# Kernel optimization log

Hardware: AMD Instinct MI355X
Metric: run time of the kernel (lower is better)

Reference implementation:

```python
import jax, jax.numpy as jnp
import numpy as np
from jax import lax

B, S, V, E, H, NH = 32, 512, 30000, 300, 200, 4
ENC = 2 * H           # bidirectional encoder size = 400
DH = ENC // NH        # head dim = 100
BUDGET = 20.0         # percent of length kept by sparseMAP
SCALING = 1.0 / 0.001 # eval-mode temperature (module sets 0.001 at test time)
NEG = -1e9


def setup_inputs():
    key = jax.random.key(0)
    ks = jax.random.split(key, 16)
    lengths = jax.random.randint(ks[0], (B,), S // 2, S + 1)
    mask = jnp.arange(S)[None, :] < lengths[:, None]          # prefix mask [B,S]
    x = jax.random.randint(ks[1], (B, S), 0, V)
    p = lambda k, sh: jax.random.normal(k, sh, jnp.float32) * 0.05
    return {
        "x": x, "mask": mask,
        "embed_table": p(ks[2], (V, E)),
        "w_ih_f": p(ks[3], (4 * H, E)), "w_hh_f": p(ks[4], (4 * H, H)), "b_f": jnp.zeros((4 * H,), jnp.float32),
        "w_ih_b": p(ks[5], (4 * H, E)), "w_hh_b": p(ks[6], (4 * H, H)), "b_b": jnp.zeros((4 * H,), jnp.float32),
        "q_state": p(ks[7], (ENC,)),
        "W_q": p(ks[8], (ENC, ENC)), "W_k": p(ks[9], (ENC, ENC)), "W_v": p(ks[10], (ENC, ENC)),
        "W_out": p(ks[11], (ENC, ENC)),
        "W_head": p(ks[12], (ENC, 1)), "b_head": jnp.zeros((1,), jnp.float32),
    }


def _lstm(xW, mask, W_hh):
    """Masked (packed-equivalent) LSTM. xW: [B,S,4H] precomputed input proj, mask [B,S] bool."""
    Bb, Ss, H4 = xW.shape
    Hh = H4 // 4
    def step(carry, t_in):
        h, c = carry
        g, m = t_in                             # g [B,4H], m [B,1] bool
        gates = g + h @ W_hh.T
        i, f, gg, o = jnp.split(gates, 4, axis=-1)
        c_new = jax.nn.sigmoid(f) * c + jax.nn.sigmoid(i) * jnp.tanh(gg)
        h_new = jax.nn.sigmoid(o) * jnp.tanh(c_new)
        return (jnp.where(m, h_new, h), jnp.where(m, c_new, c)), jnp.where(m, h_new, 0.0)
    init = (jnp.zeros((Bb, Hh), xW.dtype), jnp.zeros((Bb, Hh), xW.dtype))
    xs = (jnp.swapaxes(xW, 0, 1), jnp.swapaxes(mask[..., None], 0, 1))
    _, outs = lax.scan(step, init, xs)
    return jnp.swapaxes(outs, 0, 1)


def _proj_capped_simplex(theta, k):
    """SparseMAP budget QP: argmin ||mu - theta||^2 s.t. 0<=mu<=1, sum(mu)=k.
    Bisection on threshold tau (non-diff), then exact differentiable tau on the free set."""
    th = lax.stop_gradient(theta)
    lo = jnp.min(th) - 1.0
    hi = jnp.max(th)
    def body(_, ab):
        lo, hi = ab
        mid = 0.5 * (lo + hi)
        too_big = jnp.sum(jnp.clip(th - mid, 0.0, 1.0)) > k
        return (jnp.where(too_big, mid, lo), jnp.where(too_big, hi, mid))
    lo, hi = lax.fori_loop(0, 60, body, (lo, hi))
    tau0 = 0.5 * (lo + hi)
    mu0 = th - tau0
    free = (mu0 > 0.0) & (mu0 < 1.0)
    nU = jnp.sum(mu0 >= 1.0).astype(theta.dtype)
    nS = jnp.sum(free).astype(theta.dtype)
    tau = (jnp.sum(jnp.where(free, theta, 0.0)) + nU - k) / jnp.maximum(nS, 1.0)
    tau = jnp.where(nS > 0, tau, tau0)
    return jnp.clip(theta - tau, 0.0, 1.0)


def _forward(x, mask, embed_table, w_ih_f, w_hh_f, b_f, w_ih_b, w_hh_b, b_b,
             q_state, W_q, W_k, W_v, W_out, W_head, b_head):
    lengths = mask.sum(1)                                   # [B] int
    emb = embed_table[x]                                    # [B,S,E] (dropout off: eval)
    # forward direction
    h_f = _lstm(emb @ w_ih_f.T + b_f, mask, w_hh_f)         # [B,S,H]
    # backward direction: reverse each sample within its length (packed semantics)
    t = jnp.arange(S)
    idx = jnp.clip(lengths[:, None] - 1 - t[None, :], 0, S - 1)   # [B,S], involution on valid part
    emb_rev = jnp.take_along_axis(emb, idx[..., None], axis=1)
    h_b_rev = _lstm(emb_rev @ w_ih_b.T + b_b, mask, w_hh_b)
    h_b = jnp.take_along_axis(h_b_rev, idx[..., None], axis=1)
    h_b = jnp.where(mask[..., None], h_b, 0.0)
    h = jnp.concatenate([h_f, h_b], axis=-1)                # [B,S,ENC]
    # Hopfield pooling with learned query state, per-sample sparseMAP top-k budget
    q = (q_state @ W_q).reshape(NH, DH)                     # learned pooling query
    K = (h @ W_k).reshape(B, S, NH, DH)
    Vv = (h @ W_v).reshape(B, S, NH, DH)
    scores = SCALING * jnp.einsum('hd,bshd->bhs', q, K)     # [B,NH,S]
    scores = jnp.where(mask[:, None, :], scores, NEG)
    kbud = jnp.round(BUDGET / 100.0 * lengths.astype(jnp.float32))   # per-sample budget
    proj = jax.vmap(jax.vmap(_proj_capped_simplex, (0, None)), (0, 0))
    p = proj(scores, kbud)                                  # [B,NH,S] sparse marginals
    pooled = jnp.einsum('bhs,bshd->bhd', p, Vv).reshape(B, ENC) @ W_out
    y = jax.nn.sigmoid(pooled @ W_head + b_head)            # [B,1]
    z = jnp.where(mask, p.mean(1), 0.0)                     # [B,S] rationale
    return y, z


def reference(x, mask, embed_table, w_ih_f, w_hh_f, b_f, w_ih_b, w_hh_b, b_b,
              q_state, W_q, W_k, W_v, W_out, W_head, b_head):
    return _forward(x, mask, embed_table, w_ih_f, w_hh_f, b_f, w_ih_b, w_hh_b, b_b,
                    q_state, W_q, W_k, W_v, W_out, W_head, b_head)
```

## Files before the change

### kernel.cpp

```cpp
#include <hip/hip_runtime.h>
#include <hip/hip_bf16.h>
#include <math.h>

#define B_   32
#define S_   512
#define V_   30000
#define E_   300
#define H_   200
#define NH_  4
#define ENC_ 400
#define G4_  800
#define NEGV  (-1e9f)
#define SCALE_ 1000.0f

typedef _Float16 half2v __attribute__((ext_vector_type(2)));

#if defined(__has_builtin)
#if __has_builtin(__builtin_amdgcn_fdot2)
#define FDOT2(a,b,c) __builtin_amdgcn_fdot2((a),(b),(c),false)
#endif
#endif
#ifndef FDOT2
#define FDOT2(a,b,c) fmaf((float)(a)[1],(float)(b)[1], fmaf((float)(a)[0],(float)(b)[0],(c)))
#endif

#define OF_QVEC  320000ull
#define OF_WKQ   320448ull
#define OF_THETA 322048ull
#define OF_MU    387584ull
#define OF_HP    453120ull
#define OF_LEN   504320ull
#define OF_XWF   504384ull
#define OF_XWB   13611584ull
#define OF_HF    26718784ull
#define OF_HB    29995584ull

__global__ void k_lengths(const void* __restrict__ mask, int* __restrict__ lengths) {
  int b = blockIdx.x, lane = threadIdx.x;
  const unsigned char* mb = (const unsigned char*)mask;
  int mode;
  if (mb[1] != 0) mode = 0;
  else if (((const int*)mask)[1] != 0) mode = 1;
  else mode = 2;
  int cnt = 0;
  for (int s = lane; s < S_; s += 64) {
    int v;
    if (mode == 0)      v = mb[b*S_ + s] ? 1 : 0;
    else if (mode == 1) v = ((const int*)mask)[b*S_ + s] ? 1 : 0;
    else                v = ((const long long*)mask)[b*S_ + s] ? 1 : 0;
    cnt += v;
  }
  for (int off = 32; off; off >>= 1) cnt += __shfl_xor(cnt, off);
  if (lane == 0) lengths[b] = cnt;
}

__global__ void k_qvec(const float* __restrict__ qs, const float* __restrict__ Wq,
                       float* __restrict__ qvec) {
  __shared__ float qsl[ENC_];
  int t = threadIdx.x;
  if (t < ENC_) qsl[t] = qs[t];
  __syncthreads();
  if (t < ENC_) {
    float acc = 0.f;
    for (int i = 0; i < ENC_; ++i) acc += qsl[i] * Wq[(size_t)i*ENC_ + t];
    qvec[t] = acc;
  }
}

__global__ void k_wkq(const float* __restrict__ Wk, const float* __restrict__ qvec,
                      float* __restrict__ wkq) {
  int t = threadIdx.x;
  int e = blockIdx.x*64 + (t >> 2);
  int head = t & 3;
  if (e < ENC_) {
    float acc = 0.f;
    const float* row = Wk + (size_t)e*ENC_ + head*100;
    const float* qv  = qvec + head*100;
    for (int d = 0; d < 100; ++d) acc += row[d]*qv[d];
    wkq[e*4 + head] = acc;
  }
}

__global__ __launch_bounds__(256) void k_gemm_in(
    const int* __restrict__ x, const float* __restrict__ emb,
    const float* __restrict__ wf, const float* __restrict__ wb,
    const float* __restrict__ bf, const float* __restrict__ bb,
    float* __restrict__ xWf, float* __restrict__ xWb)
{
  __shared__ int xid[128];
  __shared__ __align__(16) float sA[16][128];
  __shared__ __align__(16) float sB[16][64];
  const int t = threadIdx.x;
  const int row0 = blockIdx.x * 128;
  const int col0 = blockIdx.y * 64;
  if (t < 128) xid[t] = x[row0 + t];
  __syncthreads();
  float acc[8][4];
  #pragma unroll
  for (int i = 0; i < 8; ++i)
    #pragma unroll
    for (int j = 0; j < 4; ++j) acc[i][j] = 0.f;
  const int y = t >> 4, xq = t & 15;
  const int rl = t >> 1, half = t & 1;
  const int cb = t & 63, kq = t >> 6;
  const int colg_b = col0 + cb;
  const float* wsrc = (colg_b < 800) ? (wf + (size_t)colg_b*300)
                                     : (wb + (size_t)(colg_b-800)*300);
  const float* asrc = emb + (size_t)xid[rl]*300;
  for (int kc = 0; kc < 19; ++kc) {
    const int k0 = kc*16;
    {
      const int kb = k0 + half*8;
      const float* src = asrc + kb;
      if (kb + 7 < 300) {
        float4 a  = *(const float4*)(src);
        float4 b4 = *(const float4*)(src+4);
        sA[half*8+0][rl]=a.x;  sA[half*8+1][rl]=a.y;  sA[half*8+2][rl]=a.z;  sA[half*8+3][rl]=a.w;
        sA[half*8+4][rl]=b4.x; sA[half*8+5][rl]=b4.y; sA[half*8+6][rl]=b4.z; sA[half*8+7][rl]=b4.w;
      } else {
        #pragma unroll
        for (int i = 0; i < 8; ++i) sA[half*8+i][rl] = (kb+i < 300) ? src[i] : 0.f;
      }
    }
    {
      const int kb = k0 + kq*4;
      if (kb + 3 < 300) {
        float4 w4 = *(const float4*)(wsrc + kb);
        sB[kq*4+0][cb]=w4.x; sB[kq*4+1][cb]=w4.y; sB[kq*4+2][cb]=w4.z; sB[kq*4+3][cb]=w4.w;
      } else {
        #pragma unroll
        for (int i = 0; i < 4; ++i) sB[kq*4+i][cb] = (kb+i < 300) ? wsrc[kb+i] : 0.f;
      }
    }
    __syncthreads();
    #pragma unroll
    for (int k = 0; k < 16; ++k) {
      float4 a0 = *(const float4*)&sA[k][y*8];
      float4 a1 = *(const float4*)&sA[k][y*8+4];
      float4 b4 = *(const float4*)&sB[k][xq*4];
      float av[8] = {a0.x,a0.y,a0.z,a0.w,a1.x,a1.y,a1.z,a1.w};
      float bv[4] = {b4.x,b4.y,b4.z,b4.w};
      #pragma unroll
      for (int i = 0; i < 8; ++i)
        #pragma unroll
        for (int j = 0; j < 4; ++j) acc[i][j] += av[i]*bv[j];
    }
    __syncthreads();
  }
  const int colg = col0 + xq*4;
  const bool isF = (colg < 800);
  const int colo = isF ? colg : (colg - 800);
  float4 bias = isF ? *(const float4*)(bf + colo) : *(const float4*)(bb + colo);
  float* dst = isF ? xWf : xWb;
  #pragma unroll
  for (int i = 0; i < 8; ++i) {
    int row = row0 + y*8 + i;
    float4 o = {acc[i][0]+bias.x, acc[i][1]+bias.y, acc[i][2]+bias.z, acc[i][3]+bias.w};
    *(float4*)(dst + (size_t)row*800 + colo) = o;
  }
}

__global__ __launch_bounds__(512, 2) void k_lstm_ws(
    const float* __restrict__ xWf, const float* __restrict__ xWb,
    const float* __restrict__ whhf, const float* __restrict__ whhb,
    const int* __restrict__ lengths,
    float* __restrict__ h_f, float* __restrict__ h_b)
{
  const int bid = blockIdx.x;
  const int dir = bid >> 5, b = bid & 31;
  const float* __restrict__ xW  = dir ? xWb : xWf;
  const float* __restrict__ whh = dir ? whhb : whhf;
  float* __restrict__ hout      = dir ? h_b : h_f;
  const int len = lengths[b];
  const int t = threadIdx.x;

  __shared__ __align__(16) _Float16 hb[256];
  __shared__ float sums[1024];

  half2v w0[100], w1[100];
  {
    const float* r0p = whh + (size_t)t*H_;
    #pragma unroll
    for (int j = 0; j < 50; ++j) {
      float4 a = *(const float4*)(r0p + 4*j);
      w0[2*j]   = half2v{(_Float16)a.x, (_Float16)a.y};
      w0[2*j+1] = half2v{(_Float16)a.z, (_Float16)a.w};
    }
    if (t < 288) {
      const float* r1p = whh + (size_t)(512+t)*H_;
      #pragma unroll
      for (int j = 0; j < 50; ++j) {
        float4 a = *(const float4*)(r1p + 4*j);
        w1[2*j]   = half2v{(_Float16)a.x, (_Float16)a.y};
        w1[2*j+1] = half2v{(_Float16)a.z, (_Float16)a.w};
      }
    } else {
      #pragma unroll
      for (int j = 0; j < 100; ++j) w1[j] = half2v{(_Float16)0.f, (_Float16)0.f};
    }
  }

  if (t < 256) hb[t] = (_Float16)0.f;
  float cst = 0.f;
  __syncthreads();

  for (int step = 0; step < len; ++step) {
    const int pos = dir ? (len-1-step) : step;
    float xi=0.f, xf=0.f, xg=0.f, xo=0.f;
    if (t < H_) {
      const float* xr = xW + ((size_t)b*S_ + pos)*G4_ + t;
      xi = xr[0]; xf = xr[H_]; xg = xr[2*H_]; xo = xr[3*H_];
    }
    float a0 = 0.f, a1 = 0.f;
    #pragma unroll
    for (int j = 0; j < 25; ++j) {
      float4 h4 = *(const float4*)&hb[8*j];
      half2v p0 = __builtin_bit_cast(half2v, h4.x);
      half2v p1 = __builtin_bit_cast(half2v, h4.y);
      half2v p2 = __builtin_bit_cast(half2v, h4.z);
      half2v p3 = __builtin_bit_cast(half2v, h4.w);
      a0 = FDOT2(w0[4*j],   p0, a0);
      a0 = FDOT2(w0[4*j+1], p1, a0);
      a0 = FDOT2(w0[4*j+2], p2, a0);
      a0 = FDOT2(w0[4*j+3], p3, a0);
      a1 = FDOT2(w1[4*j],   p0, a1);
      a1 = FDOT2(w1[4*j+1], p1, a1);
      a1 = FDOT2(w1[4*j+2], p2, a1);
      a1 = FDOT2(w1[4*j+3], p3, a1);
    }
    sums[t] = a0;
    sums[512+t] = a1;
    __syncthreads();
    if (t < H_) {
      float gi = sums[t]        + xi;
      float gf = sums[H_ + t]   + xf;
      float gg = sums[2*H_ + t] + xg;
      float go = sums[3*H_ + t] + xo;
      float ig = 1.f/(1.f+__expf(-gi));
      float fg = 1.f/(1.f+__expf(-gf));
      float og = 1.f/(1.f+__expf(-go));
      float ggc = fminf(fmaxf(gg, -10.f), 10.f);
      float eg = __expf(2.f*ggc);
      cst = fg*cst + ig*((eg-1.f)/(eg+1.f));
      float cc = fminf(fmaxf(cst, -10.f), 10.f);
      float ec = __expf(2.f*cc);
      float hn = og*((ec-1.f)/(ec+1.f));
      hout[((size_t)b*S_ + pos)*H_ + t] = hn;
      hb[t] = (_Float16)hn;
    }
    __syncthreads();
  }
}

__global__ __launch_bounds__(256) void k_scores(
    const float* __restrict__ hf, const float* __restrict__ hb,
    const float* __restrict__ wkq, const int* __restrict__ lengths,
    float* __restrict__ theta)
{
  int wid = blockIdx.x*4 + (threadIdx.x >> 6);
  int lane = threadIdx.x & 63;
  int b = wid >> 9, s = wid & 511;
  const float* hfr = hf + ((size_t)b*S_ + s)*H_;
  const float* hbr = hb + ((size_t)b*S_ + s)*H_;
  float a0=0.f, a1=0.f, a2=0.f, a3=0.f;
  for (int e = lane; e < ENC_; e += 64) {
    float hv = (e < H_) ? hfr[e] : hbr[e-H_];
    float4 w = *(const float4*)(wkq + e*4);
    a0 += hv*w.x; a1 += hv*w.y; a2 += hv*w.z; a3 += hv*w.w;
  }
  for (int off = 32; off; off >>= 1) {
    a0 += __shfl_xor(a0, off); a1 += __shfl_xor(a1, off);
    a2 += __shfl_xor(a2, off); a3 += __shfl_xor(a3, off);
  }
  if (lane == 0) {
    bool valid = s < lengths[b];
    size_t base = (size_t)b*2048 + s;
    theta[base       ] = valid ? SCALE_*a0 : NEGV;
    theta[base +  512] = valid ? SCALE_*a1 : NEGV;
    theta[base + 1024] = valid ? SCALE_*a2 : NEGV;
    theta[base + 1536] = valid ? SCALE_*a3 : NEGV;
  }
}

__global__ void k_sparsemap(const float* __restrict__ theta, const int* __restrict__ lengths,
                            float* __restrict__ mu) {
  int pid = blockIdx.x;
  int lane = threadIdx.x;
  const float* th = theta + (size_t)pid*512;
  float v[8];
  #pragma unroll
  for (int i = 0; i < 8; ++i) v[i] = th[i*64 + lane];
  float kf = rintf(0.2f * (float)lengths[pid >> 2]);
  float mn = v[0], mx = v[0];
  #pragma unroll
  for (int i = 1; i < 8; ++i) { mn = fminf(mn, v[i]); mx = fmaxf(mx, v[i]); }
  for (int off = 32; off; off >>= 1) {
    mn = fminf(mn, __shfl_xor(mn, off)); mx = fmaxf(mx, __shfl_xor(mx, off));
  }
  float lo = mn - 1.f, hi = mx;
  for (int it = 0; it < 60; ++it) {
    float mid = 0.5f*(lo + hi);
    float s = 0.f;
    #pragma unroll
    for (int i = 0; i < 8; ++i) s += fminf(fmaxf(v[i]-mid, 0.f), 1.f);
    for (int off = 32; off; off >>= 1) s += __shfl_xor(s, off);
    bool big = s > kf;
    lo = big ? mid : lo;
    hi = big ? hi : mid;
  }
  float tau0 = 0.5f*(lo + hi);
  float fs = 0.f, nU = 0.f, nS = 0.f;
  #pragma unroll
  for (int i = 0; i < 8; ++i) {
    float m0 = v[i] - tau0;
    if (m0 >= 1.f) nU += 1.f;
    else if (m0 > 0.f) { fs += v[i]; nS += 1.f; }
  }
  for (int off = 32; off; off >>= 1) {
    fs += __shfl_xor(fs, off); nU += __shfl_xor(nU, off); nS += __shfl_xor(nS, off);
  }
  float tau = (fs + nU - kf) / fmaxf(nS, 1.f);
  tau = (nS > 0.f) ? tau : tau0;
  float* mo = mu + (size_t)pid*512;
  #pragma unroll
  for (int i = 0; i < 8; ++i) mo[i*64 + lane] = fminf(fmaxf(v[i]-tau, 0.f), 1.f);
}

__global__ __launch_bounds__(512) void k_hp(
    const float* __restrict__ mu, const float* __restrict__ hf,
    const float* __restrict__ hb, float* __restrict__ hp)
{
  __shared__ float mul[512];
  int pid = blockIdx.x, b = pid >> 2;
  int t = threadIdx.x;
  mul[t] = mu[(size_t)pid*512 + t];
  __syncthreads();
  if (t < ENC_) {
    const float* hsrc = (t < H_) ? (hf + t) : (hb + (t - H_));
    float acc = 0.f;
    for (int s = 0; s < 512; ++s) {
      float m = mul[s];
      if (m != 0.f) acc += m * hsrc[((size_t)b*S_ + s)*H_];
    }
    hp[(size_t)pid*ENC_ + t] = acc;
  }
}

__global__ __launch_bounds__(512) void k_head(
    const float* __restrict__ hp, const float* __restrict__ Wv,
    const float* __restrict__ Wout, const float* __restrict__ Wh,
    const float* __restrict__ bh, float* __restrict__ out)
{
  __shared__ float hpl[1600];
  __shared__ float ppl[ENC_];
  __shared__ float ojl[ENC_];
  __shared__ float red[512];
  int b = blockIdx.x, t = threadIdx.x;
  for (int i = t; i < 1600; i += 512) hpl[i] = hp[(size_t)b*1600 + i];
  __syncthreads();
  if (t < ENC_) {
    int head = t / 100;
    float acc = 0.f;
    for (int e = 0; e < ENC_; ++e) acc += hpl[head*ENC_ + e] * Wv[(size_t)e*ENC_ + t];
    ppl[t] = acc;
  }
  __syncthreads();
  if (t < ENC_) {
    float acc = 0.f;
    for (int c = 0; c < ENC_; ++c) acc += ppl[c] * Wout[(size_t)c*ENC_ + t];
    ojl[t] = acc;
  }
  __syncthreads();
  red[t] = (t < ENC_) ? ojl[t]*Wh[t] : 0.f;
  __syncthreads();
  for (int sft = 256; sft; sft >>= 1) {
    if (t < sft) red[t] += red[t+sft];
    __syncthreads();
  }
  if (t == 0) out[b] = 1.f/(1.f + expf(-(red[0] + bh[0])));
}

__global__ void k_z(const float* __restrict__ mu, const int* __restrict__ lengths,
                    float* __restrict__ out) {
  int idx = blockIdx.x*256 + threadIdx.x;
  int b = idx >> 9, s = idx & 511;
  float zz = 0.f;
  if (s < lengths[b]) {
    size_t base = (size_t)b*2048 + s;
    zz = 0.25f*(mu[base] + mu[base+512] + mu[base+1024] + mu[base+1536]);
  }
  out[32 + idx] = zz;
}

extern "C" void kernel_launch(void* const* d_in, const int* in_sizes, int n_in,
                              void* d_out, int out_size, void* d_ws, size_t ws_size,
                              hipStream_t stream) {
  const int*   x    = (const int*)d_in[0];
  const void*  mask = d_in[1];
  const float* emb  = (const float*)d_in[2];
  const float* wihf = (const float*)d_in[3];
  const float* whhf = (const float*)d_in[4];
  const float* bf   = (const float*)d_in[5];
  const float* wihb = (const float*)d_in[6];
  const float* whhb = (const float*)d_in[7];
  const float* bb   = (const float*)d_in[8];
  const float* qs   = (const float*)d_in[9];
  const float* Wq   = (const float*)d_in[10];
  const float* Wk   = (const float*)d_in[11];
  const float* Wv   = (const float*)d_in[12];
  const float* Wout = (const float*)d_in[13];
  const float* Wh   = (const float*)d_in[14];
  const float* bh   = (const float*)d_in[15];
  float* out = (float*)d_out;
  float* W = (float*)d_ws;
  int* lengths = (int*)(W + OF_LEN);

  k_lengths<<<32, 64, 0, stream>>>(mask, lengths);
  k_qvec<<<1, 512, 0, stream>>>(qs, Wq, W+OF_QVEC);
  k_wkq<<<7, 256, 0, stream>>>(Wk, W+OF_QVEC, W+OF_WKQ);
  hipMemsetAsync(W+OF_HF, 0, (size_t)B_*S_*H_*sizeof(float), stream);
  hipMemsetAsync(W+OF_HB, 0, (size_t)B_*S_*H_*sizeof(float), stream);
  k_gemm_in<<<dim3(128, 25), 256, 0, stream>>>(x, emb, wihf, wihb, bf, bb,
                                               W+OF_XWF, W+OF_XWB);
  k_lstm_ws<<<64, 512, 0, stream>>>(W+OF_XWF, W+OF_XWB, whhf, whhb,
                                    lengths, W+OF_HF, W+OF_HB);
  k_scores<<<4096, 256, 0, stream>>>(W+OF_HF, W+OF_HB, W+OF_WKQ, lengths, W+OF_THETA);
  k_sparsemap<<<128, 64, 0, stream>>>(W+OF_THETA, lengths, W+OF_MU);
  k_hp<<<128, 512, 0, stream>>>(W+OF_MU, W+OF_HF, W+OF_HB, W+OF_HP);
  k_head<<<32, 512, 0, stream>>>(W+OF_HP, Wv, Wout, Wh, bh, out);
  k_z<<<64, 256, 0, stream>>>(W+OF_MU, lengths, out);
}
```

Baseline: 966.1 us.

## Use MFMA for input GEMM, one-gate-per-thread LSTM, drop h memsets

The input projection GEMM now converts embeddings and weights to fp16 in shared memory and runs on 16x16x32 MFMA instructions instead of scalar FMAs. The recurrent LSTM kernel moves to 1024-thread blocks in which each of 800 threads owns one gate row. That thread computes the dot product with two accumulators and applies its own sigmoid or tanh, which shortens the serial per-step critical path. The memsets that zeroed the hidden-state buffers are removed, and the scores kernel skips the dot product for padded positions. The trade-offs are lower input-projection precision and the chance that uninitialized padded hidden rows are read downstream.

```diff
diff --git a/kernel.cpp b/kernel.cpp
--- a/kernel.cpp
+++ b/kernel.cpp
@@ -14,6 +14,8 @@
 #define SCALE_ 1000.0f
 
 typedef _Float16 half2v __attribute__((ext_vector_type(2)));
+typedef _Float16 f16x8  __attribute__((ext_vector_type(8)));
+typedef float    f32x4  __attribute__((ext_vector_type(4)));
 
 #if defined(__has_builtin)
 #if __has_builtin(__builtin_amdgcn_fdot2)
@@ -81,86 +83,97 @@
   }
 }
 
-__global__ __launch_bounds__(256) void k_gemm_in(
+__global__ __launch_bounds__(256) void k_gemm_mfma(
     const int* __restrict__ x, const float* __restrict__ emb,
     const float* __restrict__ wf, const float* __restrict__ wb,
     const float* __restrict__ bf, const float* __restrict__ bb,
     float* __restrict__ xWf, float* __restrict__ xWb)
 {
   __shared__ int xid[128];
-  __shared__ __align__(16) float sA[16][128];
-  __shared__ __align__(16) float sB[16][64];
+  __shared__ __align__(16) _Float16 sA[128][40];
+  __shared__ __align__(16) _Float16 sB[64][40];
   const int t = threadIdx.x;
   const int row0 = blockIdx.x * 128;
   const int col0 = blockIdx.y * 64;
   if (t < 128) xid[t] = x[row0 + t];
-  __syncthreads();
-  float acc[8][4];
-  #pragma unroll
-  for (int i = 0; i < 8; ++i)
-    #pragma unroll
-    for (int j = 0; j < 4; ++j) acc[i][j] = 0.f;
-  const int y = t >> 4, xq = t & 15;
-  const int rl = t >> 1, half = t & 1;
-  const int cb = t & 63, kq = t >> 6;
-  const int colg_b = col0 + cb;
-  const float* wsrc = (colg_b < 800) ? (wf + (size_t)colg_b*300)
-                                     : (wb + (size_t)(colg_b-800)*300);
-  const float* asrc = emb + (size_t)xid[rl]*300;
-  for (int kc = 0; kc < 19; ++kc) {
-    const int k0 = kc*16;
+  const int w = t >> 6, lane = t & 63;
+  const int wr = w >> 1, wc = w & 1;
+  f32x4 acc[4][2] = {};
+  const int ar = t >> 1, ah = t & 1;
+  const int bc = t >> 2, bq = t & 3;
+  const int colg = col0 + bc;
+  const float* wsrc = (colg < 800) ? (wf + (size_t)colg*300)
+                                   : (wb + (size_t)(colg-800)*300);
+  __syncthreads();
+  const float* asrc = emb + (size_t)xid[ar]*300;
+  for (int kc = 0; kc < 10; ++kc) {
+    const int k0 = kc*32;
     {
-      const int kb = k0 + half*8;
-      const float* src = asrc + kb;
-      if (kb + 7 < 300) {
-        float4 a  = *(const float4*)(src);
-        float4 b4 = *(const float4*)(src+4);
-        sA[half*8+0][rl]=a.x;  sA[half*8+1][rl]=a.y;  sA[half*8+2][rl]=a.z;  sA[half*8+3][rl]=a.w;
-        sA[half*8+4][rl]=b4.x; sA[half*8+5][rl]=b4.y; sA[half*8+6][rl]=b4.z; sA[half*8+7][rl]=b4.w;
+      const int kb = k0 + ah*16;
+      _Float16 tmp[16];
+      if (kb + 15 < 300) {
+        #pragma unroll
+        for (int q = 0; q < 4; ++q) {
+          float4 a = *(const float4*)(asrc + kb + 4*q);
+          tmp[4*q]  =(_Float16)a.x; tmp[4*q+1]=(_Float16)a.y;
+          tmp[4*q+2]=(_Float16)a.z; tmp[4*q+3]=(_Float16)a.w;
+        }
       } else {
         #pragma unroll
-        for (int i = 0; i < 8; ++i) sA[half*8+i][rl] = (kb+i < 300) ? src[i] : 0.f;
-      }
+        for (int i = 0; i < 16; ++i)
+          tmp[i] = (_Float16)((kb+i < 300) ? asrc[kb+i] : 0.f);
+      }
+      *(f16x8*)&sA[ar][ah*16]   = *(f16x8*)&tmp[0];
+      *(f16x8*)&sA[ar][ah*16+8] = *(f16x8*)&tmp[8];
     }
     {
-      const int kb = k0 + kq*4;
-      if (kb + 3 < 300) {
-        float4 w4 = *(const float4*)(wsrc + kb);
-        sB[kq*4+0][cb]=w4.x; sB[kq*4+1][cb]=w4.y; sB[kq*4+2][cb]=w4.z; sB[kq*4+3][cb]=w4.w;
+      const int kb = k0 + bq*8;
+      _Float16 tmp[8];
+      if (kb + 7 < 300) {
+        #pragma unroll
+        for (int q = 0; q < 2; ++q) {
+          float4 a = *(const float4*)(wsrc + kb + 4*q);
+          tmp[4*q]  =(_Float16)a.x; tmp[4*q+1]=(_Float16)a.y;
+          tmp[4*q+2]=(_Float16)a.z; tmp[4*q+3]=(_Float16)a.w;
+        }
       } else {
         #pragma unroll
-        for (int i = 0; i < 4; ++i) sB[kq*4+i][cb] = (kb+i < 300) ? wsrc[kb+i] : 0.f;
-      }
+        for (int i = 0; i < 8; ++i)
+          tmp[i] = (_Float16)((kb+i < 300) ? wsrc[kb+i] : 0.f);
+      }
+      *(f16x8*)&sB[bc][bq*8] = *(f16x8*)&tmp[0];
     }
     __syncthreads();
+    const int fr = lane & 15, kg = lane >> 4;
+    f16x8 b0 = *(const f16x8*)&sB[wc*32 + fr][kg*8];
+    f16x8 b1 = *(const f16x8*)&sB[wc*32 + 16 + fr][kg*8];
     #pragma unroll
-    for (int k = 0; k < 16; ++k) {
-      float4 a0 = *(const float4*)&sA[k][y*8];
-      float4 a1 = *(const float4*)&sA[k][y*8+4];
-      float4 b4 = *(const float4*)&sB[k][xq*4];
-      float av[8] = {a0.x,a0.y,a0.z,a0.w,a1.x,a1.y,a1.z,a1.w};
-      float bv[4] = {b4.x,b4.y,b4.z,b4.w};
+    for (int m = 0; m < 4; ++m) {
+      f16x8 afrag = *(const f16x8*)&sA[wr*64 + m*16 + fr][kg*8];
+      acc[m][0] = __builtin_amdgcn_mfma_f32_16x16x32_f16(afrag, b0, acc[m][0], 0,0,0);
+      acc[m][1] = __builtin_amdgcn_mfma_f32_16x16x32_f16(afrag, b1, acc[m][1], 0,0,0);
+    }
+    __syncthreads();
+  }
+  const int crb = (lane >> 4) * 4, ccol = lane & 15;
+  #pragma unroll
+  for (int n = 0; n < 2; ++n) {
+    int colg2 = col0 + wc*32 + n*16 + ccol;
+    bool isF = colg2 < 800;
+    int colo = isF ? colg2 : colg2 - 800;
+    float bias = isF ? bf[colo] : bb[colo];
+    float* dst = isF ? xWf : xWb;
+    #pragma unroll
+    for (int m = 0; m < 4; ++m) {
+      int row = row0 + wr*64 + m*16 + crb;
       #pragma unroll
-      for (int i = 0; i < 8; ++i)
-        #pragma unroll
-        for (int j = 0; j < 4; ++j) acc[i][j] += av[i]*bv[j];
-    }
-    __syncthreads();
-  }
-  const int colg = col0 + xq*4;
-  const bool isF = (colg < 800);
-  const int colo = isF ? colg : (colg - 800);
-  float4 bias = isF ? *(const float4*)(bf + colo) : *(const float4*)(bb + colo);
-  float* dst = isF ? xWf : xWb;
-  #pragma unroll
-  for (int i = 0; i < 8; ++i) {
-    int row = row0 + y*8 + i;
-    float4 o = {acc[i][0]+bias.x, acc[i][1]+bias.y, acc[i][2]+bias.z, acc[i][3]+bias.w};
-    *(float4*)(dst + (size_t)row*800 + colo) = o;
-  }
-}
-
-__global__ __launch_bounds__(512, 2) void k_lstm_ws(
+      for (int r = 0; r < 4; ++r)
+        dst[(size_t)(row+r)*800 + colo] = acc[m][n][r] + bias;
+    }
+  }
+}
+
+__global__ __launch_bounds__(1024) void k_lstm_v2(
     const float* __restrict__ xWf, const float* __restrict__ xWb,
     const float* __restrict__ whhf, const float* __restrict__ whhb,
     const int* __restrict__ lengths,
@@ -173,80 +186,82 @@
   float* __restrict__ hout      = dir ? h_b : h_f;
   const int len = lengths[b];
   const int t = threadIdx.x;
-
-  __shared__ __align__(16) _Float16 hb[256];
-  __shared__ float sums[1024];
-
-  half2v w0[100], w1[100];
-  {
-    const float* r0p = whh + (size_t)t*H_;
+  const int active = (t < G4_);
+
+  __shared__ __align__(16) _Float16 hbh[200];
+  __shared__ float gact[G4_];
+
+  half2v w[100];
+  if (active) {
+    const float* rp = whh + (size_t)t*H_;
     #pragma unroll
     for (int j = 0; j < 50; ++j) {
-      float4 a = *(const float4*)(r0p + 4*j);
-      w0[2*j]   = half2v{(_Float16)a.x, (_Float16)a.y};
-      w0[2*j+1] = half2v{(_Float16)a.z, (_Float16)a.w};
-    }
-    if (t < 288) {
-      const float* r1p = whh + (size_t)(512+t)*H_;
-      #pragma unroll
-      for (int j = 0; j < 50; ++j) {
-        float4 a = *(const float4*)(r1p + 4*j);
-        w1[2*j]   = half2v{(_Float16)a.x, (_Float16)a.y};
-        w1[2*j+1] = half2v{(_Float16)a.z, (_Float16)a.w};
-      }
-    } else {
-      #pragma unroll
-      for (int j = 0; j < 100; ++j) w1[j] = half2v{(_Float16)0.f, (_Float16)0.f};
-    }
-  }
-
-  if (t < 256) hb[t] = (_Float16)0.f;
+      float2 a = *(const float2*)(rp + 2*j);
+      w[j] = half2v{(_Float16)a.x, (_Float16)a.y};
+    }
+    #pragma unroll
+    for (int j = 0; j < 50; ++j) {
+      float2 a = *(const float2*)(rp + 100 + 2*j);
+      w[50+j] = half2v{(_Float16)a.x, (_Float16)a.y};
+    }
+  }
+  if (t < 200) hbh[t] = (_Float16)0.f;
   float cst = 0.f;
+  const float* xbase = xW + (size_t)b*S_*G4_;
+  const int isTanh = (t >= 400) && (t < 600);
   __syncthreads();
 
   for (int step = 0; step < len; ++step) {
     const int pos = dir ? (len-1-step) : step;
-    float xi=0.f, xf=0.f, xg=0.f, xo=0.f;
-    if (t < H_) {
-      const float* xr = xW + ((size_t)b*S_ + pos)*G4_ + t;
-      xi = xr[0]; xf = xr[H_]; xg = xr[2*H_]; xo = xr[3*H_];
-    }
-    float a0 = 0.f, a1 = 0.f;
-    #pragma unroll
-    for (int j = 0; j < 25; ++j) {
-      float4 h4 = *(const float4*)&hb[8*j];
-      half2v p0 = __builtin_bit_cast(half2v, h4.x);
-      half2v p1 = __builtin_bit_cast(half2v, h4.y);
-      half2v p2 = __builtin_bit_cast(half2v, h4.z);
-      half2v p3 = __builtin_bit_cast(half2v, h4.w);
-      a0 = FDOT2(w0[4*j],   p0, a0);
-      a0 = FDOT2(w0[4*j+1], p1, a0);
-      a0 = FDOT2(w0[4*j+2], p2, a0);
-      a0 = FDOT2(w0[4*j+3], p3, a0);
-      a1 = FDOT2(w1[4*j],   p0, a1);
-      a1 = FDOT2(w1[4*j+1], p1, a1);
-      a1 = FDOT2(w1[4*j+2], p2, a1);
-      a1 = FDOT2(w1[4*j+3], p3, a1);
-    }
-    sums[t] = a0;
-    sums[512+t] = a1;
+    if (active) {
+      float xv = xbase[(size_t)pos*G4_ + t];
+      float a0 = 0.f, a1 = 0.f;
+      #pragma unroll
+      for (int j = 0; j < 12; ++j) {
+        float4 h4 = *(const float4*)&hbh[8*j];
+        a0 = FDOT2(w[4*j],   __builtin_bit_cast(half2v, h4.x), a0);
+        a1 = FDOT2(w[4*j+1], __builtin_bit_cast(half2v, h4.y), a1);
+        a0 = FDOT2(w[4*j+2], __builtin_bit_cast(half2v, h4.z), a0);
+        a1 = FDOT2(w[4*j+3], __builtin_bit_cast(half2v, h4.w), a1);
+      }
+      {
+        float2 h2 = *(const float2*)&hbh[96];
+        a0 = FDOT2(w[48], __builtin_bit_cast(half2v, h2.x), a0);
+        a1 = FDOT2(w[49], __builtin_bit_cast(half2v, h2.y), a1);
+      }
+      #pragma unroll
+      for (int j = 0; j < 12; ++j) {
+        float4 h4 = *(const float4*)&hbh[100 + 8*j];
+        a0 = FDOT2(w[50+4*j],   __builtin_bit_cast(half2v, h4.x), a0);
+        a1 = FDOT2(w[50+4*j+1], __builtin_bit_cast(half2v, h4.y), a1);
+        a0 = FDOT2(w[50+4*j+2], __builtin_bit_cast(half2v, h4.z), a0);
+        a1 = FDOT2(w[50+4*j+3], __builtin_bit_cast(half2v, h4.w), a1);
+      }
+      {
+        float2 h2 = *(const float2*)&hbh[196];
+        a0 = FDOT2(w[98], __builtin_bit_cast(half2v, h2.x), a0);
+        a1 = FDOT2(w[99], __builtin_bit_cast(half2v, h2.y), a1);
+      }
+      float pre = a0 + a1 + xv;
+      float act;
+      if (isTanh) {
+        float gc = fminf(fmaxf(pre, -10.f), 10.f);
+        float e2 = __expf(2.f*gc);
+        act = (e2-1.f)/(e2+1.f);
+      } else {
+        act = 1.f/(1.f+__expf(-pre));
+      }
+      gact[t] = act;
+    }
     __syncthreads();
-    if (t < H_) {
-      float gi = sums[t]        + xi;
-      float gf = sums[H_ + t]   + xf;
-      float gg = sums[2*H_ + t] + xg;
-      float go = sums[3*H_ + t] + xo;
-      float ig = 1.f/(1.f+__expf(-gi));
-      float fg = 1.f/(1.f+__expf(-gf));
-      float og = 1.f/(1.f+__expf(-go));
-      float ggc = fminf(fmaxf(gg, -10.f), 10.f);
-      float eg = __expf(2.f*ggc);
-      cst = fg*cst + ig*((eg-1.f)/(eg+1.f));
+    if (t < 200) {
+      float ig = gact[t], fg = gact[200+t], gg = gact[400+t], og = gact[600+t];
+      cst = fg*cst + ig*gg;
       float cc = fminf(fmaxf(cst, -10.f), 10.f);
       float ec = __expf(2.f*cc);
       float hn = og*((ec-1.f)/(ec+1.f));
       hout[((size_t)b*S_ + pos)*H_ + t] = hn;
-      hb[t] = (_Float16)hn;
+      hbh[t] = (_Float16)hn;
     }
     __syncthreads();
   }
@@ -262,18 +277,20 @@
   int b = wid >> 9, s = wid & 511;
   const float* hfr = hf + ((size_t)b*S_ + s)*H_;
   const float* hbr = hb + ((size_t)b*S_ + s)*H_;
+  bool valid = s < lengths[b];
   float a0=0.f, a1=0.f, a2=0.f, a3=0.f;
-  for (int e = lane; e < ENC_; e += 64) {
-    float hv = (e < H_) ? hfr[e] : hbr[e-H_];
-    float4 w = *(const float4*)(wkq + e*4);
-    a0 += hv*w.x; a1 += hv*w.y; a2 += hv*w.z; a3 += hv*w.w;
-  }
-  for (int off = 32; off; off >>= 1) {
-    a0 += __shfl_xor(a0, off); a1 += __shfl_xor(a1, off);
-    a2 += __shfl_xor(a2, off); a3 += __shfl_xor(a3, off);
+  if (valid) {
+    for (int e = lane; e < ENC_; e += 64) {
+      float hv = (e < H_) ? hfr[e] : hbr[e-H_];
+      float4 w = *(const float4*)(wkq + e*4);
+      a0 += hv*w.x; a1 += hv*w.y; a2 += hv*w.z; a3 += hv*w.w;
+    }
+    for (int off = 32; off; off >>= 1) {
+      a0 += __shfl_xor(a0, off); a1 += __shfl_xor(a1, off);
+      a2 += __shfl_xor(a2, off); a3 += __shfl_xor(a3, off);
+    }
   }
   if (lane == 0) {
-    bool valid = s < lengths[b];
     size_t base = (size_t)b*2048 + s;
     theta[base       ] = valid ? SCALE_*a0 : NEGV;
     theta[base +  512] = valid ? SCALE_*a1 : NEGV;
@@ -418,12 +435,10 @@
   k_lengths<<<32, 64, 0, stream>>>(mask, lengths);
   k_qvec<<<1, 512, 0, stream>>>(qs, Wq, W+OF_QVEC);
   k_wkq<<<7, 256, 0, stream>>>(Wk, W+OF_QVEC, W+OF_WKQ);
-  hipMemsetAsync(W+OF_HF, 0, (size_t)B_*S_*H_*sizeof(float), stream);
-  hipMemsetAsync(W+OF_HB, 0, (size_t)B_*S_*H_*sizeof(float), stream);
-  k_gemm_in<<<dim3(128, 25), 256, 0, stream>>>(x, emb, wihf, wihb, bf, bb,
-                                               W+OF_XWF, W+OF_XWB);
-  k_lstm_ws<<<64, 512, 0, stream>>>(W+OF_XWF, W+OF_XWB, whhf, whhb,
-                                    lengths, W+OF_HF, W+OF_HB);
+  k_gemm_mfma<<<dim3(128, 25), 256, 0, stream>>>(x, emb, wihf, wihb, bf, bb,
+                                                 W+OF_XWF, W+OF_XWB);
+  k_lstm_v2<<<64, 1024, 0, stream>>>(W+OF_XWF, W+OF_XWB, whhf, whhb,
+                                     lengths, W+OF_HF, W+OF_HB);
   k_scores<<<4096, 256, 0, stream>>>(W+OF_HF, W+OF_HB, W+OF_WKQ, lengths, W+OF_THETA);
   k_sparsemap<<<128, 64, 0, stream>>>(W+OF_THETA, lengths, W+OF_MU);
   k_hp<<<128, 512, 0, stream>>>(W+OF_MU, W+OF_HF, W+OF_HB, W+OF_HP);
```

After: 877.6 us. 9.2% less time.
